# Performance work log

Measured on AMD Instinct MI355X. Metric: run time of the kernel, lower is better.

## Reference

```python
import jax, jax.numpy as jnp
import numpy as np

B, S, H, V, E, C = 32, 512, 512, 32000, 768, 3
D = E + C  # LSTM input dim = embedding + one-hot prior


def setup_inputs() -> dict:
    key = jax.random.key(0)
    ks = jax.random.split(key, 13)
    p = lambda k, shape: (jax.random.normal(k, shape, jnp.float32) * 0.02)
    return {
        "embedding_table": p(ks[0], (V, E)),
        "fwd_kernel": p(ks[1], (D, 4 * H)),
        "fwd_rec_kernel": p(ks[2], (H, 4 * H)),
        "fwd_bias": p(ks[3], (4 * H,)),
        "bwd_kernel": p(ks[4], (D, 4 * H)),
        "bwd_rec_kernel": p(ks[5], (H, 4 * H)),
        "bwd_bias": p(ks[6], (4 * H,)),
        "w1": p(ks[7], (2 * H, H)),
        "b1": jnp.zeros((H,), jnp.float32),
        "w2": p(ks[8], (H, C)),
        "b2": jnp.zeros((C,), jnp.float32),
        "input_ids": jax.random.randint(ks[9], (B, S), 0, V),
        "prior_info": jax.random.randint(ks[10], (B, S), 0, C),
        "labels": jax.random.randint(ks[11], (B, S), 0, C),
    }


def _lstm(x, K, R, b, reverse):
    """Keras-style LSTM (gate order i,f,c,o). x: [B,S,D] -> [B,S,H].
    With reverse=True, lax.scan processes time backwards and emits outputs
    aligned to original positions, matching Keras Bidirectional's
    go_backwards + output re-reversal."""
    zx = jnp.einsum('bsd,dh->bsh', x, K) + b  # input projection, [B,S,4H]
    zx = jnp.swapaxes(zx, 0, 1)               # [S,B,4H]
    h0 = jnp.zeros((x.shape[0], R.shape[0]), x.dtype)

    def step(carry, z):
        h, c = carry
        z = z + h @ R
        i, f, g, o = jnp.split(z, 4, axis=-1)
        c = jax.nn.sigmoid(f) * c + jax.nn.sigmoid(i) * jnp.tanh(g)
        h = jax.nn.sigmoid(o) * jnp.tanh(c)
        return (h, c), h

    _, ys = jax.lax.scan(step, (h0, h0), zx, reverse=reverse)
    return jnp.swapaxes(ys, 0, 1)  # [B,S,H]


def reference(embedding_table, fwd_kernel, fwd_rec_kernel, fwd_bias,
              bwd_kernel, bwd_rec_kernel, bwd_bias,
              w1, b1, w2, b2, input_ids, prior_info, labels):
    emb = embedding_table[input_ids]                       # [B,S,E] gather
    prior = jax.nn.one_hot(prior_info, C, dtype=emb.dtype)  # [B,S,3]
    x = jnp.concatenate([emb, prior], axis=-1)             # [B,S,771]
    hf = _lstm(x, fwd_kernel, fwd_rec_kernel, fwd_bias, reverse=False)
    hb = _lstm(x, bwd_kernel, bwd_rec_kernel, bwd_bias, reverse=True)
    h = jnp.concatenate([hf, hb], axis=-1)                 # [B,S,2H]
    h = h @ w1 + b1                                        # Dense (linear)
    logits = h @ w2 + b2                                   # [B,S,3]
    probs = jax.nn.softmax(logits, axis=-1)
    logp = jax.nn.log_softmax(logits, axis=-1)
    lab = jax.nn.one_hot(labels, C, dtype=logp.dtype)
    loss = jnp.mean(-jnp.sum(logp * lab, axis=(-1, -2)))
    return probs, loss
```

## Files before the change

### kernel.cpp

```cpp
#include <hip/hip_runtime.h>
#include <hip/hip_bf16.h>

#define BB 32
#define SS 512
#define HH 512
#define VV 32000
#define EE 768
#define NC 3
#define G4 2048
#define MM (BB*SS)
#define SENT 0xFFFFFFFFu

typedef __attribute__((ext_vector_type(8))) short bf16x8;
typedef __attribute__((ext_vector_type(4))) float f32x4;
typedef unsigned int u32;
typedef unsigned short u16;
typedef __attribute__((ext_vector_type(4))) u32 u32x4;
typedef __attribute__((ext_vector_type(2))) u32 u32x2;

#define MFMA(a,b,c) __builtin_amdgcn_mfma_f32_16x16x32_bf16(a,b,c,0,0,0)

static __device__ __forceinline__ u16 f2bf(float f) {
  union { float f; u32 u; } v; v.f = f;
  return (u16)((v.u + 0x7fffu + ((v.u >> 16) & 1u)) >> 16);
}
static __device__ __forceinline__ float bf2f(u16 h) {
  union { u32 u; float f; } v; v.u = ((u32)h) << 16;
  return v.f;
}
static __device__ __forceinline__ float sigm(float x) { return 1.f/(1.f+__expf(-x)); }
static __device__ __forceinline__ float tanh_f(float x) {
  x = fminf(8.f, fmaxf(-8.f, x));
  float t = __expf(2.f*x);
  return (t-1.f)/(t+1.f);
}
static __device__ __forceinline__ bool ok16(u32 v) {
  return ((v & 0xFFFFu) != 0xFFFFu) && ((v >> 16) != 0xFFFFu);
}

__global__ void k_conv(const float* __restrict__ src, u16* __restrict__ dst, int n8) {
  int i = blockIdx.x * blockDim.x + threadIdx.x;
  if (i >= n8) return;
  const float4* s = ((const float4*)src) + (size_t)i*2;
  float4 a = s[0], b = s[1];
  u32 x = (u32)f2bf(a.x) | ((u32)f2bf(a.y) << 16);
  u32 y = (u32)f2bf(a.z) | ((u32)f2bf(a.w) << 16);
  u32 z = (u32)f2bf(b.x) | ((u32)f2bf(b.y) << 16);
  u32 w = (u32)f2bf(b.z) | ((u32)f2bf(b.w) << 16);
  ((uint4*)dst)[i] = make_uint4(x, y, z, w);
}

__global__ void k_pack(const float* __restrict__ src, u16* __restrict__ dst, int K, int N) {
  int tid = blockIdx.x * 256 + threadIdx.x;
  int nkf = K >> 5;
  int l = tid & 63, fi = tid >> 6;
  int kf = fi % nkf, nf = fi / nkf;
  if (nf >= (N >> 4)) return;
  int col = nf * 16 + (l & 15);
  int k0 = kf * 32 + (l >> 4) * 8;
  u32 o[4];
  #pragma unroll
  for (int j = 0; j < 4; ++j) {
    u16 lo = f2bf(src[(size_t)(k0 + 2*j) * N + col]);
    u16 hi = f2bf(src[(size_t)(k0 + 2*j + 1) * N + col]);
    o[j] = (u32)lo | ((u32)hi << 16);
  }
  *((uint4*)(dst + (size_t)tid * 8)) = make_uint4(o[0], o[1], o[2], o[3]);
}

static __device__ __forceinline__ void proj_role(
    int pid,
    const u16* __restrict__ embT, const u16* __restrict__ Kfp, const u16* __restrict__ Kbp,
    const float* __restrict__ fb, const float* __restrict__ bb,
    const float* __restrict__ fK, const float* __restrict__ bK,
    const int* __restrict__ ids, const int* __restrict__ prior,
    u16* __restrict__ zxf, u16* __restrict__ zxb)
{
  int w = threadIdx.x >> 6, l = threadIdx.x & 63;
  for (int wk = pid; wk < 4096; wk += 224) {
    int kk = wk >> 5, gy = wk & 31;
    int mt = (kk & 1) ? (127 - (kk >> 1)) : (kk >> 1);
    int dir = gy >> 4, nt = gy & 15;
    const u16* Bp = dir ? Kbp : Kfp;
    const float* bias = dir ? bb : fb;
    const float* Kp = (dir ? bK : fK) + (size_t)EE * G4;
    u16* zx = dir ? zxb : zxf;
    int m0 = mt * 128 + w * 32;
    int r0 = m0 + (l & 15);
    int id0 = ids[(r0 & 31) * SS + (r0 >> 5)];
    int id1 = ids[((r0 + 16) & 31) * SS + ((r0 + 16) >> 5)];
    const u16* a0p = embT + (size_t)id0 * EE + (l >> 4) * 8;
    const u16* a1p = embT + (size_t)id1 * EE + (l >> 4) * 8;
    f32x4 acc[2][8];
    #pragma unroll
    for (int i = 0; i < 2; ++i)
      #pragma unroll
      for (int j = 0; j < 8; ++j) acc[i][j] = (f32x4){0.f,0.f,0.f,0.f};
    const u16* bbase = Bp + ((size_t)(nt*8)*24)*512 + (size_t)l*8;
    for (int kf = 0; kf < 24; ++kf) {
      bf16x8 a0 = *(const bf16x8*)(a0p + kf*32);
      bf16x8 a1 = *(const bf16x8*)(a1p + kf*32);
      #pragma unroll
      for (int nf = 0; nf < 8; ++nf) {
        bf16x8 bv = *(const bf16x8*)(bbase + (size_t)(nf*24 + kf)*512);
        acc[0][nf] = MFMA(a0, bv, acc[0][nf]);
        acc[1][nf] = MFMA(a1, bv, acc[1][nf]);
      }
    }
    int cb = nt*128 + (l & 15);
    #pragma unroll
    for (int mi = 0; mi < 2; ++mi) {
      #pragma unroll
      for (int r = 0; r < 4; ++r) {
        int row = m0 + mi*16 + (l >> 4)*4 + r;
        int p = prior[(row & 31) * SS + (row >> 5)];
        const float* kr = Kp + (size_t)p * G4;
        u16* zr = zx + (size_t)row * G4;
        #pragma unroll
        for (int nf = 0; nf < 8; ++nf) {
          int col = cb + nf*16;
          u32 v = (u32)f2bf(acc[mi][nf][r] + bias[col] + kr[col]);
          asm volatile("global_store_short %0, %1, off sc0 sc1"
                       :: "v"(zr + col), "v"(v) : "memory");
        }
      }
    }
  }
}

__global__ __launch_bounds__(256, 1) void k_fused(
    const u16* __restrict__ embT, const u16* __restrict__ Kfp, const u16* __restrict__ Kbp,
    const float* __restrict__ fb, const float* __restrict__ bb,
    const float* __restrict__ fK, const float* __restrict__ bK,
    const int* __restrict__ ids, const int* __restrict__ prior,
    u16* __restrict__ zxf, u16* __restrict__ zxb,
    const u16* __restrict__ Rf, const u16* __restrict__ Rb,
    u16* __restrict__ hf, u16* __restrict__ hb)
{
  __shared__ char hstage[32*1040];
  __shared__ float zbuf[4][32][33];

  int wg = blockIdx.x;
  if (wg >= 32) {
    proj_role(wg - 32, embT, Kfp, Kbp, fb, bb, fK, bK, ids, prior, zxf, zxb);
    return;
  }
  int dir = wg >> 4, wgi = wg & 15;
  const u16* zx = dir ? zxb : zxf;
  const u16* Rp = dir ? Rb : Rf;
  u16* hbuf = dir ? hb : hf;
  int tid = threadIdx.x;
  int g = tid >> 6, l = tid & 63;
  int ncb0 = g*32 + wgi*2;
  bf16x8 rb0[16], rb1[16];
  #pragma unroll
  for (int kf = 0; kf < 16; ++kf) {
    rb0[kf] = *(const bf16x8*)(Rp + (((size_t)ncb0*16 + kf)*64 + l)*8);
    rb1[kf] = *(const bf16x8*)(Rp + (((size_t)(ncb0+1)*16 + kf)*64 + l)*8);
  }

  int eb = tid >> 3;
  int ecb = (tid & 7) * 4;
  const char* sread0 = hstage + (l & 15)*1040 + (l >> 4)*16;
  const char* sread1 = sread0 + 16*1040;
  char* swrite = hstage + (tid >> 3)*1040 + (tid & 7)*16;
  size_t goff = (size_t)(tid >> 3)*1024 + (tid & 7)*16;

  float c0 = 0.f, c1 = 0.f, c2 = 0.f, c3 = 0.f;
  for (int step = 0; step < SS; ++step) {
    int t = dir ? (SS - 1 - step) : step;
    const char* zxp = (const char*)(zx + ((size_t)t*BB + eb)*G4 + wgi*32 + ecb);
    u32x2 xi, xfv, xgv, xov;
    #define LDZ(r, off) asm volatile("global_load_dwordx2 %0, %1, off " off " sc0 sc1" \
                                     : "=v"(r) : "v"(zxp) : "memory")
    f32x4 a00 = {0.f,0.f,0.f,0.f}, a01 = {0.f,0.f,0.f,0.f};
    f32x4 a10 = {0.f,0.f,0.f,0.f}, a11 = {0.f,0.f,0.f,0.f};
    if (step > 0) {
      int tp = dir ? t + 1 : t - 1;
      const char* gsrc = (const char*)(hbuf + (size_t)tp*BB*HH) + goff;
      u32x4 S0, S1, S2, S3, S4, S5, S6, S7;
      #define LDC(r, off) asm volatile("global_load_dwordx4 %0, %1, off " off " sc0 sc1" \
                                       : "=v"(r) : "v"(gsrc) : "memory")
      for (;;) {
        LDZ(xi, "");  LDZ(xfv, "offset:1024");
        LDZ(xgv, "offset:2048"); LDZ(xov, "offset:3072");
        LDC(S0, "");            LDC(S1, "offset:128");
        LDC(S2, "offset:256");  LDC(S3, "offset:384");
        LDC(S4, "offset:512");  LDC(S5, "offset:640");
        LDC(S6, "offset:768");  LDC(S7, "offset:896");
        asm volatile("s_waitcnt vmcnt(0)" ::: "memory");
        __builtin_amdgcn_sched_barrier(0);
        bool ok = ok16(xi[0]) && ok16(xi[1]) && ok16(xfv[0]) && ok16(xfv[1])
               && ok16(xgv[0]) && ok16(xgv[1]) && ok16(xov[0]) && ok16(xov[1])
               && S0[0]!=SENT && S0[1]!=SENT && S0[2]!=SENT && S0[3]!=SENT
               && S1[0]!=SENT && S1[1]!=SENT && S1[2]!=SENT && S1[3]!=SENT
               && S2[0]!=SENT && S2[1]!=SENT && S2[2]!=SENT && S2[3]!=SENT
               && S3[0]!=SENT && S3[1]!=SENT && S3[2]!=SENT && S3[3]!=SENT
               && S4[0]!=SENT && S4[1]!=SENT && S4[2]!=SENT && S4[3]!=SENT
               && S5[0]!=SENT && S5[1]!=SENT && S5[2]!=SENT && S5[3]!=SENT
               && S6[0]!=SENT && S6[1]!=SENT && S6[2]!=SENT && S6[3]!=SENT
               && S7[0]!=SENT && S7[1]!=SENT && S7[2]!=SENT && S7[3]!=SENT;
        if (__all(ok)) break;
        __builtin_amdgcn_s_sleep(1);
      }
      #undef LDC
      __builtin_amdgcn_sched_barrier(0);
      *(u32x4*)(swrite)       = S0;
      *(u32x4*)(swrite + 128) = S1;
      *(u32x4*)(swrite + 256) = S2;
      *(u32x4*)(swrite + 384) = S3;
      *(u32x4*)(swrite + 512) = S4;
      *(u32x4*)(swrite + 640) = S5;
      *(u32x4*)(swrite + 768) = S6;
      *(u32x4*)(swrite + 896) = S7;
      __syncthreads();
      #pragma unroll
      for (int kf = 0; kf < 16; ++kf) {
        bf16x8 f0 = *(const bf16x8*)(sread0 + kf*64);
        bf16x8 f1 = *(const bf16x8*)(sread1 + kf*64);
        a00 = MFMA(f0, rb0[kf], a00);
        a01 = MFMA(f0, rb1[kf], a01);
        a10 = MFMA(f1, rb0[kf], a10);
        a11 = MFMA(f1, rb1[kf], a11);
      }
    } else {
      for (;;) {
        LDZ(xi, "");  LDZ(xfv, "offset:1024");
        LDZ(xgv, "offset:2048"); LDZ(xov, "offset:3072");
        asm volatile("s_waitcnt vmcnt(0)" ::: "memory");
        __builtin_amdgcn_sched_barrier(0);
        bool ok = ok16(xi[0]) && ok16(xi[1]) && ok16(xfv[0]) && ok16(xfv[1])
               && ok16(xgv[0]) && ok16(xgv[1]) && ok16(xov[0]) && ok16(xov[1]);
        if (__all(ok)) break;
        __builtin_amdgcn_s_sleep(1);
      }
      __builtin_amdgcn_sched_barrier(0);
    }
    #undef LDZ
    int zc = l & 15;
    int zr = (l >> 4) * 4;
    #pragma unroll
    for (int r = 0; r < 4; ++r) {
      zbuf[g][zc][zr + r]           = a00[r];
      zbuf[g][16 + zc][zr + r]      = a01[r];
      zbuf[g][zc][16 + zr + r]      = a10[r];
      zbuf[g][16 + zc][16 + zr + r] = a11[r];
    }
    __syncthreads();
    float z0[4], z1[4], z2[4], z3[4];
    #pragma unroll
    for (int j = 0; j < 4; ++j) {
      z0[j] = zbuf[0][ecb + j][eb];
      z1[j] = zbuf[1][ecb + j][eb];
      z2[j] = zbuf[2][ecb + j][eb];
      z3[j] = zbuf[3][ecb + j][eb];
    }
    z0[0] += bf2f((u16)(xi[0] & 0xffffu)); z0[1] += bf2f((u16)(xi[0] >> 16));
    z0[2] += bf2f((u16)(xi[1] & 0xffffu)); z0[3] += bf2f((u16)(xi[1] >> 16));
    z1[0] += bf2f((u16)(xfv[0] & 0xffffu)); z1[1] += bf2f((u16)(xfv[0] >> 16));
    z1[2] += bf2f((u16)(xfv[1] & 0xffffu)); z1[3] += bf2f((u16)(xfv[1] >> 16));
    z2[0] += bf2f((u16)(xgv[0] & 0xffffu)); z2[1] += bf2f((u16)(xgv[0] >> 16));
    z2[2] += bf2f((u16)(xgv[1] & 0xffffu)); z2[3] += bf2f((u16)(xgv[1] >> 16));
    z3[0] += bf2f((u16)(xov[0] & 0xffffu)); z3[1] += bf2f((u16)(xov[0] >> 16));
    z3[2] += bf2f((u16)(xov[1] & 0xffffu)); z3[3] += bf2f((u16)(xov[1] >> 16));
    c0 = sigm(z1[0])*c0 + sigm(z0[0])*tanh_f(z2[0]);
    c1 = sigm(z1[1])*c1 + sigm(z0[1])*tanh_f(z2[1]);
    c2 = sigm(z1[2])*c2 + sigm(z0[2])*tanh_f(z2[2]);
    c3 = sigm(z1[3])*c3 + sigm(z0[3])*tanh_f(z2[3]);
    float h0 = sigm(z3[0])*tanh_f(c0);
    float h1 = sigm(z3[1])*tanh_f(c1);
    float h2 = sigm(z3[2])*tanh_f(c2);
    float h3 = sigm(z3[3])*tanh_f(c3);
    u32x2 hpk;
    hpk[0] = (u32)f2bf(h0) | ((u32)f2bf(h1) << 16);
    hpk[1] = (u32)f2bf(h2) | ((u32)f2bf(h3) << 16);
    u16* hp = hbuf + ((size_t)t*BB + eb)*HH + wgi*32 + ecb;
    asm volatile("global_store_dwordx2 %0, %1, off sc0 sc1" :: "v"(hp), "v"(hpk) : "memory");
  }
}

__global__ __launch_bounds__(256) void k_dense(
    const u16* __restrict__ hf, const u16* __restrict__ hb,
    const u16* __restrict__ w1p, const float* __restrict__ b1,
    u16* __restrict__ h1)
{
  int mt = blockIdx.x, nt = blockIdx.y;
  int w = threadIdx.x >> 6, l = threadIdx.x & 63;
  int m0 = mt*128 + w*32;
  int r0 = m0 + (l & 15);
  const u16* f0 = hf + (size_t)r0*HH + (l >> 4)*8;
  const u16* f1 = hf + (size_t)(r0+16)*HH + (l >> 4)*8;
  const u16* g0 = hb + (size_t)r0*HH + (l >> 4)*8;
  const u16* g1 = hb + (size_t)(r0+16)*HH + (l >> 4)*8;
  f32x4 acc[2][8];
  #pragma unroll
  for (int i = 0; i < 2; ++i)
    #pragma unroll
    for (int j = 0; j < 8; ++j) acc[i][j] = (f32x4){0.f,0.f,0.f,0.f};
  const u16* bbase = w1p + ((size_t)(nt*8)*32)*512 + (size_t)l*8;
  for (int kf = 0; kf < 32; ++kf) {
    const u16* s0 = (kf < 16) ? (f0 + kf*32) : (g0 + (kf-16)*32);
    const u16* s1 = (kf < 16) ? (f1 + kf*32) : (g1 + (kf-16)*32);
    bf16x8 a0 = *(const bf16x8*)s0;
    bf16x8 a1 = *(const bf16x8*)s1;
    #pragma unroll
    for (int nf = 0; nf < 8; ++nf) {
      bf16x8 bv = *(const bf16x8*)(bbase + (size_t)(nf*32 + kf)*512);
      acc[0][nf] = MFMA(a0, bv, acc[0][nf]);
      acc[1][nf] = MFMA(a1, bv, acc[1][nf]);
    }
  }
  int cb = nt*128 + (l & 15);
  #pragma unroll
  for (int mi = 0; mi < 2; ++mi) {
    #pragma unroll
    for (int r = 0; r < 4; ++r) {
      int row = m0 + mi*16 + (l >> 4)*4 + r;
      #pragma unroll
      for (int nf = 0; nf < 8; ++nf) {
        int col = cb + nf*16;
        h1[(size_t)row*HH + col] = f2bf(acc[mi][nf][r] + b1[col]);
      }
    }
  }
}

__global__ __launch_bounds__(256) void k_out(
    const u16* __restrict__ h1, const float* __restrict__ w2, const float* __restrict__ b2,
    const int* __restrict__ labels, float* __restrict__ out, float* __restrict__ part)
{
  int w = threadIdx.x >> 6, l = threadIdx.x & 63;
  float w2r[8][3];
  #pragma unroll
  for (int i = 0; i < 8; ++i)
    #pragma unroll
    for (int c = 0; c < 3; ++c) w2r[i][c] = w2[(l*8 + i)*3 + c];
  float b20 = b2[0], b21 = b2[1], b22 = b2[2];
  float nll = 0.f;
  int base = (blockIdx.x*4 + w)*16;
  for (int r = 0; r < 16; ++r) {
    int row = base + r;
    bf16x8 hv = *(const bf16x8*)(h1 + (size_t)row*HH + l*8);
    float s0 = 0.f, s1 = 0.f, s2 = 0.f;
    #pragma unroll
    for (int i = 0; i < 8; ++i) {
      float x = bf2f((u16)hv[i]);
      s0 += x*w2r[i][0]; s1 += x*w2r[i][1]; s2 += x*w2r[i][2];
    }
    #pragma unroll
    for (int off = 32; off > 0; off >>= 1) {
      s0 += __shfl_down(s0, off);
      s1 += __shfl_down(s1, off);
      s2 += __shfl_down(s2, off);
    }
    if (l == 0) {
      float l0 = s0+b20, l1 = s1+b21, l2 = s2+b22;
      float m = fmaxf(l0, fmaxf(l1, l2));
      float e0 = __expf(l0-m), e1 = __expf(l1-m), e2 = __expf(l2-m);
      float Z = e0+e1+e2, inv = 1.f/Z;
      int b = row & 31, s = row >> 5;
      float* po = out + ((size_t)b*SS + s)*3;
      po[0] = e0*inv; po[1] = e1*inv; po[2] = e2*inv;
      int lab = labels[b*SS + s];
      float ll = (lab == 0) ? l0 : (lab == 1 ? l1 : l2);
      nll += (m + __logf(Z)) - ll;
    }
  }
  __shared__ float ps[4];
  if (l == 0) ps[w] = nll;
  __syncthreads();
  if (threadIdx.x == 0) part[blockIdx.x] = ps[0]+ps[1]+ps[2]+ps[3];
}

__global__ void k_loss(const float* __restrict__ part, float* __restrict__ out) {
  __shared__ float sh[256];
  sh[threadIdx.x] = part[threadIdx.x];
  __syncthreads();
  for (int s = 128; s > 0; s >>= 1) {
    if (threadIdx.x < s) sh[threadIdx.x] += sh[threadIdx.x + s];
    __syncthreads();
  }
  if (threadIdx.x == 0) out[(size_t)MM*NC] = sh[0] / (float)BB;
}

extern "C" void kernel_launch(void* const* d_in, const int* in_sizes, int n_in,
                              void* d_out, int out_size, void* d_ws, size_t ws_size,
                              hipStream_t stream) {
  (void)in_sizes; (void)n_in; (void)out_size;
  const float* emb = (const float*)d_in[0];
  const float* fK  = (const float*)d_in[1];
  const float* fR  = (const float*)d_in[2];
  const float* fb  = (const float*)d_in[3];
  const float* bK  = (const float*)d_in[4];
  const float* bR  = (const float*)d_in[5];
  const float* bb  = (const float*)d_in[6];
  const float* w1  = (const float*)d_in[7];
  const float* b1  = (const float*)d_in[8];
  const float* w2  = (const float*)d_in[9];
  const float* b2  = (const float*)d_in[10];
  const int* ids   = (const int*)d_in[11];
  const int* prior = (const int*)d_in[12];
  const int* labels= (const int*)d_in[13];

  size_t off = 0;
  auto take = [&](size_t bytes) -> char* {
    char* p = (char*)d_ws + off;
    off += (bytes + 255) & ~(size_t)255;
    return p;
  };
  u16* embT = (u16*)take((size_t)VV*EE*2);
  u16* Kfp  = (u16*)take((size_t)EE*G4*2);
  u16* Kbp  = (u16*)take((size_t)EE*G4*2);
  u16* Rfp  = (u16*)take((size_t)HH*G4*2);
  u16* Rbp  = (u16*)take((size_t)HH*G4*2);
  u16* w1p  = (u16*)take((size_t)(2*HH)*HH*2);
  u16* zxf  = (u16*)take((size_t)MM*G4*2);
  u16* zxb  = (u16*)take((size_t)MM*G4*2);
  u16* hf   = (u16*)take((size_t)MM*HH*2);
  u16* hb   = (u16*)take((size_t)MM*HH*2);
  u16* h1   = (u16*)take((size_t)MM*HH*2);
  float* part = (float*)take(256*4);
  if (off > ws_size) return;

  hipMemsetAsync(zxf, 0xFF, (size_t)MM*G4*2, stream);
  hipMemsetAsync(zxb, 0xFF, (size_t)MM*G4*2, stream);
  hipMemsetAsync(hf, 0xFF, (size_t)MM*HH*2, stream);
  hipMemsetAsync(hb, 0xFF, (size_t)MM*HH*2, stream);
  k_conv<<<12000, 256, 0, stream>>>(emb, embT, VV*EE/8);
  k_pack<<<768, 256, 0, stream>>>(fK, Kfp, EE, G4);
  k_pack<<<768, 256, 0, stream>>>(bK, Kbp, EE, G4);
  k_pack<<<512, 256, 0, stream>>>(fR, Rfp, HH, G4);
  k_pack<<<512, 256, 0, stream>>>(bR, Rbp, HH, G4);
  k_pack<<<256, 256, 0, stream>>>(w1, w1p, 2*HH, HH);
  k_fused<<<256, 256, 0, stream>>>(embT, Kfp, Kbp, fb, bb, fK, bK, ids, prior,
                                   zxf, zxb, Rfp, Rbp, hf, hb);
  k_dense<<<dim3(128,4), 256, 0, stream>>>(hf, hb, w1p, b1, h1);
  k_out<<<256, 256, 0, stream>>>(h1, w2, b2, labels, (float*)d_out, part);
  k_loss<<<1, 256, 0, stream>>>(part, (float*)d_out);
}
```

Baseline: 2.249 ms.

## Reorder projection output layout for contiguous per-step loads; merge prep kernels

The input-projection producer now stages results through shared memory and writes zx in a gate-interleaved layout. Each recurrent thread can then fetch its four gates with two 16-byte loads instead of four 8-byte loads, and the producer issues 8-byte stores instead of scattered 2-byte stores. Producer blocks are also split by direction, with the backward direction walking time tiles in reverse, so each direction's data arrives in the order its consumer needs it. The five conversion and packing launches are merged into one prep kernel to cut launch overhead. The cost is extra LDS use and two block barriers per producer tile.

After: 2.250 ms. Within noise of the previous version (+0.1%).

```diff
diff --git a/kernel.cpp b/kernel.cpp
--- a/kernel.cpp
+++ b/kernel.cpp
@@ -38,9 +38,9 @@
   return ((v & 0xFFFFu) != 0xFFFFu) && ((v >> 16) != 0xFFFFu);
 }
 
-__global__ void k_conv(const float* __restrict__ src, u16* __restrict__ dst, int n8) {
-  int i = blockIdx.x * blockDim.x + threadIdx.x;
-  if (i >= n8) return;
+static __device__ void conv_body(int blk, const float* __restrict__ src, u16* __restrict__ dst) {
+  int i = blk * 256 + threadIdx.x;
+  if (i >= VV*EE/8) return;
   const float4* s = ((const float4*)src) + (size_t)i*2;
   float4 a = s[0], b = s[1];
   u32 x = (u32)f2bf(a.x) | ((u32)f2bf(a.y) << 16);
@@ -49,9 +49,8 @@
   u32 w = (u32)f2bf(b.z) | ((u32)f2bf(b.w) << 16);
   ((uint4*)dst)[i] = make_uint4(x, y, z, w);
 }
-
-__global__ void k_pack(const float* __restrict__ src, u16* __restrict__ dst, int K, int N) {
-  int tid = blockIdx.x * 256 + threadIdx.x;
+static __device__ void pack_body(int blk, const float* __restrict__ src, u16* __restrict__ dst, int K, int N) {
+  int tid = blk * 256 + threadIdx.x;
   int nkf = K >> 5;
   int l = tid & 63, fi = tid >> 6;
   int kf = fi % nkf, nf = fi / nkf;
@@ -67,24 +66,40 @@
   }
   *((uint4*)(dst + (size_t)tid * 8)) = make_uint4(o[0], o[1], o[2], o[3]);
 }
+__global__ __launch_bounds__(256) void k_prep(
+    const float* emb, u16* embT,
+    const float* fK, u16* Kfp, const float* bK, u16* Kbp,
+    const float* fR, u16* Rfp, const float* bR, u16* Rbp,
+    const float* w1, u16* w1p)
+{
+  int b = blockIdx.x;
+  if      (b < 12000) conv_body(b, emb, embT);
+  else if (b < 12768) pack_body(b-12000, fK, Kfp, EE, G4);
+  else if (b < 13536) pack_body(b-12768, bK, Kbp, EE, G4);
+  else if (b < 14048) pack_body(b-13536, fR, Rfp, HH, G4);
+  else if (b < 14560) pack_body(b-14048, bR, Rbp, HH, G4);
+  else                pack_body(b-14560, w1, w1p, 2*HH, HH);
+}
 
 static __device__ __forceinline__ void proj_role(
-    int pid,
+    int pid, char* smem,
     const u16* __restrict__ embT, const u16* __restrict__ Kfp, const u16* __restrict__ Kbp,
-    const float* __restrict__ fb, const float* __restrict__ bb,
-    const float* __restrict__ fK, const float* __restrict__ bK,
+    const float* __restrict__ fb_, const float* __restrict__ bb_,
+    const float* __restrict__ fK_, const float* __restrict__ bK_,
     const int* __restrict__ ids, const int* __restrict__ prior,
-    u16* __restrict__ zxf, u16* __restrict__ zxb)
+    u16* __restrict__ zx2f, u16* __restrict__ zx2b)
 {
   int w = threadIdx.x >> 6, l = threadIdx.x & 63;
-  for (int wk = pid; wk < 4096; wk += 224) {
-    int kk = wk >> 5, gy = wk & 31;
-    int mt = (kk & 1) ? (127 - (kk >> 1)) : (kk >> 1);
-    int dir = gy >> 4, nt = gy & 15;
-    const u16* Bp = dir ? Kbp : Kfp;
-    const float* bias = dir ? bb : fb;
-    const float* Kp = (dir ? bK : fK) + (size_t)EE * G4;
-    u16* zx = dir ? zxb : zxf;
+  int dir = pid >= 112;
+  int i0 = dir ? pid - 112 : pid;
+  const u16* Bp = dir ? Kbp : Kfp;
+  const float* bias = dir ? bb_ : fb_;
+  const float* Kp = (dir ? bK_ : fK_) + (size_t)EE * G4;
+  u16* zx2 = dir ? zx2b : zx2f;
+  u16* lt = (u16*)smem;
+  for (int i = i0; i < 2048; i += 112) {
+    int mtseq = i >> 4, nt = i & 15;
+    int mt = dir ? (127 - mtseq) : mtseq;
     int m0 = mt * 128 + w * 32;
     int r0 = m0 + (l & 15);
     int id0 = ids[(r0 & 31) * SS + (r0 >> 5)];
@@ -93,9 +108,9 @@
     const u16* a1p = embT + (size_t)id1 * EE + (l >> 4) * 8;
     f32x4 acc[2][8];
     #pragma unroll
-    for (int i = 0; i < 2; ++i)
+    for (int a = 0; a < 2; ++a)
       #pragma unroll
-      for (int j = 0; j < 8; ++j) acc[i][j] = (f32x4){0.f,0.f,0.f,0.f};
+      for (int j = 0; j < 8; ++j) acc[a][j] = (f32x4){0.f,0.f,0.f,0.f};
     const u16* bbase = Bp + ((size_t)(nt*8)*24)*512 + (size_t)l*8;
     for (int kf = 0; kf < 24; ++kf) {
       bf16x8 a0 = *(const bf16x8*)(a0p + kf*32);
@@ -107,23 +122,39 @@
         acc[1][nf] = MFMA(a1, bv, acc[1][nf]);
       }
     }
-    int cb = nt*128 + (l & 15);
+    __syncthreads();
     #pragma unroll
     for (int mi = 0; mi < 2; ++mi) {
       #pragma unroll
       for (int r = 0; r < 4; ++r) {
-        int row = m0 + mi*16 + (l >> 4)*4 + r;
+        int rloc = w*32 + mi*16 + (l >> 4)*4 + r;
+        int row = mt*128 + rloc;
         int p = prior[(row & 31) * SS + (row >> 5)];
         const float* kr = Kp + (size_t)p * G4;
-        u16* zr = zx + (size_t)row * G4;
         #pragma unroll
         for (int nf = 0; nf < 8; ++nf) {
-          int col = cb + nf*16;
-          u32 v = (u32)f2bf(acc[mi][nf][r] + bias[col] + kr[col]);
-          asm volatile("global_store_short %0, %1, off sc0 sc1"
-                       :: "v"(zr + col), "v"(v) : "memory");
+          int lc = (l & 15) + nf*16;
+          int colg = nt*128 + lc;
+          lt[rloc*136 + lc] = f2bf(acc[mi][nf][r] + bias[colg] + kr[colg]);
         }
       }
+    }
+    __syncthreads();
+    int g = nt >> 2, cqb = (nt & 3) * 32;
+    int cql = threadIdx.x & 31;
+    #pragma unroll
+    for (int k = 0; k < 8; ++k) {
+      int rloc = k*16 + (threadIdx.x >> 5);
+      int s = mt*4 + (rloc >> 5);
+      int b = rloc & 31;
+      u32x2 v0 = *(const u32x2*)(lt + rloc*136 + cql*4);
+      u32x2 v1 = *(const u32x2*)(lt + (rloc+8)*136 + cql*4);
+      u16* d0 = zx2 + (((size_t)(s*BB + b)*128 + cqb + cql)*16 + g*4);
+      int rloc1 = rloc + 8;
+      int s1 = mt*4 + (rloc1 >> 5), b1 = rloc1 & 31;
+      u16* d1 = zx2 + (((size_t)(s1*BB + b1)*128 + cqb + cql)*16 + g*4);
+      asm volatile("global_store_dwordx2 %0, %1, off sc0 sc1" :: "v"(d0), "v"(v0) : "memory");
+      asm volatile("global_store_dwordx2 %0, %1, off sc0 sc1" :: "v"(d1), "v"(v1) : "memory");
     }
   }
 }
@@ -133,20 +164,21 @@
     const float* __restrict__ fb, const float* __restrict__ bb,
     const float* __restrict__ fK, const float* __restrict__ bK,
     const int* __restrict__ ids, const int* __restrict__ prior,
-    u16* __restrict__ zxf, u16* __restrict__ zxb,
+    u16* __restrict__ zx2f, u16* __restrict__ zx2b,
     const u16* __restrict__ Rf, const u16* __restrict__ Rb,
     u16* __restrict__ hf, u16* __restrict__ hb)
 {
-  __shared__ char hstage[32*1040];
-  __shared__ float zbuf[4][32][33];
+  __shared__ char smem[50176];
+  char* hstage = smem;
+  float (*zbuf)[32][33] = (float (*)[32][33])(smem + 33280);
 
   int wg = blockIdx.x;
   if (wg >= 32) {
-    proj_role(wg - 32, embT, Kfp, Kbp, fb, bb, fK, bK, ids, prior, zxf, zxb);
+    proj_role(wg - 32, smem, embT, Kfp, Kbp, fb, bb, fK, bK, ids, prior, zx2f, zx2b);
     return;
   }
   int dir = wg >> 4, wgi = wg & 15;
-  const u16* zx = dir ? zxb : zxf;
+  const u16* zx2 = dir ? zx2b : zx2f;
   const u16* Rp = dir ? Rb : Rf;
   u16* hbuf = dir ? hb : hf;
   int tid = threadIdx.x;
@@ -160,19 +192,24 @@
   }
 
   int eb = tid >> 3;
-  int ecb = (tid & 7) * 4;
+  int q = tid & 7;
+  int colq = wgi*8 + q;
   const char* sread0 = hstage + (l & 15)*1040 + (l >> 4)*16;
   const char* sread1 = sread0 + 16*1040;
-  char* swrite = hstage + (tid >> 3)*1040 + (tid & 7)*16;
-  size_t goff = (size_t)(tid >> 3)*1024 + (tid & 7)*16;
+  char* swrite = hstage + (tid >> 3)*1040 + q*16;
+  size_t goff = (size_t)(tid >> 3)*1024 + q*16;
 
   float c0 = 0.f, c1 = 0.f, c2 = 0.f, c3 = 0.f;
   for (int step = 0; step < SS; ++step) {
     int t = dir ? (SS - 1 - step) : step;
-    const char* zxp = (const char*)(zx + ((size_t)t*BB + eb)*G4 + wgi*32 + ecb);
-    u32x2 xi, xfv, xgv, xov;
-    #define LDZ(r, off) asm volatile("global_load_dwordx2 %0, %1, off " off " sc0 sc1" \
-                                     : "=v"(r) : "v"(zxp) : "memory")
+    const char* zxp = (const char*)(zx2 + ((size_t)(t*BB + eb)*128 + colq)*16);
+    u32x4 ZA, ZB;
+    #define LDZ() do { \
+      asm volatile("global_load_dwordx4 %0, %1, off sc0 sc1" : "=v"(ZA) : "v"(zxp) : "memory"); \
+      asm volatile("global_load_dwordx4 %0, %1, off offset:16 sc0 sc1" : "=v"(ZB) : "v"(zxp) : "memory"); \
+    } while(0)
+    #define ZOK (ok16(ZA[0]) && ok16(ZA[1]) && ok16(ZA[2]) && ok16(ZA[3]) \
+              && ok16(ZB[0]) && ok16(ZB[1]) && ok16(ZB[2]) && ok16(ZB[3]))
     f32x4 a00 = {0.f,0.f,0.f,0.f}, a01 = {0.f,0.f,0.f,0.f};
     f32x4 a10 = {0.f,0.f,0.f,0.f}, a11 = {0.f,0.f,0.f,0.f};
     if (step > 0) {
@@ -182,16 +219,14 @@
       #define LDC(r, off) asm volatile("global_load_dwordx4 %0, %1, off " off " sc0 sc1" \
                                        : "=v"(r) : "v"(gsrc) : "memory")
       for (;;) {
-        LDZ(xi, "");  LDZ(xfv, "offset:1024");
-        LDZ(xgv, "offset:2048"); LDZ(xov, "offset:3072");
+        LDZ();
         LDC(S0, "");            LDC(S1, "offset:128");
         LDC(S2, "offset:256");  LDC(S3, "offset:384");
         LDC(S4, "offset:512");  LDC(S5, "offset:640");
         LDC(S6, "offset:768");  LDC(S7, "offset:896");
         asm volatile("s_waitcnt vmcnt(0)" ::: "memory");
         __builtin_amdgcn_sched_barrier(0);
-        bool ok = ok16(xi[0]) && ok16(xi[1]) && ok16(xfv[0]) && ok16(xfv[1])
-               && ok16(xgv[0]) && ok16(xgv[1]) && ok16(xov[0]) && ok16(xov[1])
+        bool ok = ZOK
                && S0[0]!=SENT && S0[1]!=SENT && S0[2]!=SENT && S0[3]!=SENT
                && S1[0]!=SENT && S1[1]!=SENT && S1[2]!=SENT && S1[3]!=SENT
                && S2[0]!=SENT && S2[1]!=SENT && S2[2]!=SENT && S2[3]!=SENT
@@ -225,18 +260,16 @@
       }
     } else {
       for (;;) {
-        LDZ(xi, "");  LDZ(xfv, "offset:1024");
-        LDZ(xgv, "offset:2048"); LDZ(xov, "offset:3072");
+        LDZ();
         asm volatile("s_waitcnt vmcnt(0)" ::: "memory");
         __builtin_amdgcn_sched_barrier(0);
-        bool ok = ok16(xi[0]) && ok16(xi[1]) && ok16(xfv[0]) && ok16(xfv[1])
-               && ok16(xgv[0]) && ok16(xgv[1]) && ok16(xov[0]) && ok16(xov[1]);
-        if (__all(ok)) break;
+        if (__all(ZOK)) break;
         __builtin_amdgcn_s_sleep(1);
       }
       __builtin_amdgcn_sched_barrier(0);
     }
     #undef LDZ
+    #undef ZOK
     int zc = l & 15;
     int zr = (l >> 4) * 4;
     #pragma unroll
@@ -247,6 +280,7 @@
       zbuf[g][16 + zc][16 + zr + r] = a11[r];
     }
     __syncthreads();
+    int ecb = q * 4;
     float z0[4], z1[4], z2[4], z3[4];
     #pragma unroll
     for (int j = 0; j < 4; ++j) {
@@ -255,14 +289,14 @@
       z2[j] = zbuf[2][ecb + j][eb];
       z3[j] = zbuf[3][ecb + j][eb];
     }
-    z0[0] += bf2f((u16)(xi[0] & 0xffffu)); z0[1] += bf2f((u16)(xi[0] >> 16));
-    z0[2] += bf2f((u16)(xi[1] & 0xffffu)); z0[3] += bf2f((u16)(xi[1] >> 16));
-    z1[0] += bf2f((u16)(xfv[0] & 0xffffu)); z1[1] += bf2f((u16)(xfv[0] >> 16));
-    z1[2] += bf2f((u16)(xfv[1] & 0xffffu)); z1[3] += bf2f((u16)(xfv[1] >> 16));
-    z2[0] += bf2f((u16)(xgv[0] & 0xffffu)); z2[1] += bf2f((u16)(xgv[0] >> 16));
-    z2[2] += bf2f((u16)(xgv[1] & 0xffffu)); z2[3] += bf2f((u16)(xgv[1] >> 16));
-    z3[0] += bf2f((u16)(xov[0] & 0xffffu)); z3[1] += bf2f((u16)(xov[0] >> 16));
-    z3[2] += bf2f((u16)(xov[1] & 0xffffu)); z3[3] += bf2f((u16)(xov[1] >> 16));
+    z0[0] += bf2f((u16)(ZA[0] & 0xffffu)); z0[1] += bf2f((u16)(ZA[0] >> 16));
+    z0[2] += bf2f((u16)(ZA[1] & 0xffffu)); z0[3] += bf2f((u16)(ZA[1] >> 16));
+    z1[0] += bf2f((u16)(ZA[2] & 0xffffu)); z1[1] += bf2f((u16)(ZA[2] >> 16));
+    z1[2] += bf2f((u16)(ZA[3] & 0xffffu)); z1[3] += bf2f((u16)(ZA[3] >> 16));
+    z2[0] += bf2f((u16)(ZB[0] & 0xffffu)); z2[1] += bf2f((u16)(ZB[0] >> 16));
+    z2[2] += bf2f((u16)(ZB[1] & 0xffffu)); z2[3] += bf2f((u16)(ZB[1] >> 16));
+    z3[0] += bf2f((u16)(ZB[2] & 0xffffu)); z3[1] += bf2f((u16)(ZB[2] >> 16));
+    z3[2] += bf2f((u16)(ZB[3] & 0xffffu)); z3[3] += bf2f((u16)(ZB[3] >> 16));
     c0 = sigm(z1[0])*c0 + sigm(z0[0])*tanh_f(z2[0]);
     c1 = sigm(z1[1])*c1 + sigm(z0[1])*tanh_f(z2[1]);
     c2 = sigm(z1[2])*c2 + sigm(z0[2])*tanh_f(z2[2]);
@@ -274,7 +308,7 @@
     u32x2 hpk;
     hpk[0] = (u32)f2bf(h0) | ((u32)f2bf(h1) << 16);
     hpk[1] = (u32)f2bf(h2) | ((u32)f2bf(h3) << 16);
-    u16* hp = hbuf + ((size_t)t*BB + eb)*HH + wgi*32 + ecb;
+    u16* hp = hbuf + ((size_t)t*BB + eb)*HH + wgi*32 + q*4;
     asm volatile("global_store_dwordx2 %0, %1, off sc0 sc1" :: "v"(hp), "v"(hpk) : "memory");
   }
 }
@@ -426,12 +460,7 @@
   hipMemsetAsync(zxb, 0xFF, (size_t)MM*G4*2, stream);
   hipMemsetAsync(hf, 0xFF, (size_t)MM*HH*2, stream);
   hipMemsetAsync(hb, 0xFF, (size_t)MM*HH*2, stream);
-  k_conv<<<12000, 256, 0, stream>>>(emb, embT, VV*EE/8);
-  k_pack<<<768, 256, 0, stream>>>(fK, Kfp, EE, G4);
-  k_pack<<<768, 256, 0, stream>>>(bK, Kbp, EE, G4);
-  k_pack<<<512, 256, 0, stream>>>(fR, Rfp, HH, G4);
-  k_pack<<<512, 256, 0, stream>>>(bR, Rbp, HH, G4);
-  k_pack<<<256, 256, 0, stream>>>(w1, w1p, 2*HH, HH);
+  k_prep<<<14816, 256, 0, stream>>>(emb, embT, fK, Kfp, bK, Kbp, fR, Rfp, bR, Rbp, w1, w1p);
   k_fused<<<256, 256, 0, stream>>>(embT, Kfp, Kbp, fb, bb, fK, bK, ids, prior,
                                    zxf, zxb, Rfp, Rbp, hf, hb);
   k_dense<<<dim3(128,4), 256, 0, stream>>>(hf, hb, w1p, b1, h1);
```
